# Kernel optimization log

Measured on AMD Instinct MI355X. Metric: run time of the kernel, lower is better.

The kernel has to match this reference:

```python
import jax, jax.numpy as jnp
import numpy as np

B, S, DM, H, HD = 2, 4096, 768, 12, 64
SCALING = HD ** -0.5
LN_EPS = 1e-12
ROPE_BASE = 10000.0


def rotate_half(x):
    x1, x2 = jnp.split(x, 2, axis=-1)
    return jnp.concatenate([-x2, x1], axis=-1)


def setup_inputs() -> dict:
    key = jax.random.key(0)
    ks = jax.random.split(key, 8)
    s = 0.02
    hidden_states = jax.random.normal(ks[0], (B, S, DM), dtype=jnp.float32)
    # true rotary tables: inv_freq over head_dim/2, duplicated (HF convention)
    inv_freq = 1.0 / (ROPE_BASE ** (jnp.arange(0, HD, 2, dtype=jnp.float32) / HD))
    freqs = jnp.arange(S, dtype=jnp.float32)[:, None] * inv_freq[None, :]  # [S, HD/2]
    emb = jnp.concatenate([freqs, freqs], axis=-1)                          # [S, HD]
    cos, sin = jnp.cos(emb), jnp.sin(emb)
    return {
        "hidden_states": hidden_states,
        "cos": cos,
        "sin": sin,
        "Wq": jax.random.normal(ks[1], (DM, DM), dtype=jnp.float32) * s,
        "bq": jnp.zeros((DM,), dtype=jnp.float32),
        "Wk": jax.random.normal(ks[2], (DM, DM), dtype=jnp.float32) * s,
        "bk": jnp.zeros((DM,), dtype=jnp.float32),
        "Wv": jax.random.normal(ks[3], (DM, DM), dtype=jnp.float32) * s,
        "bv": jnp.zeros((DM,), dtype=jnp.float32),
        "Wo": jax.random.normal(ks[4], (DM, DM), dtype=jnp.float32) * s,
        "ln_g": jnp.ones((DM,), dtype=jnp.float32),
        "ln_b": jnp.zeros((DM,), dtype=jnp.float32),
    }


def reference(hidden_states, cos, sin, Wq, bq, Wk, bk, Wv, bv, Wo, ln_g, ln_b):
    # QKV projections -> [B, H, S, HD]
    def proj(W, b):
        return (hidden_states @ W.T + b).reshape(B, S, H, HD).transpose(0, 2, 1, 3)
    q, k, v = proj(Wq, bq), proj(Wk, bk), proj(Wv, bv)

    # RoPE (cos/sin broadcast over batch & heads)
    c = cos[None, None, :, :]
    s_ = sin[None, None, :, :]
    q = q * c + rotate_half(q) * s_
    k = k * c + rotate_half(k) * s_

    # Faithful to source: q pre-scaled, then eager attention scales scores again
    q = q * SCALING
    scores = jnp.einsum("bhsd,bhtd->bhst", q, k) * SCALING  # [B,H,S,S]
    probs = jax.nn.softmax(scores.astype(jnp.float32), axis=-1).astype(v.dtype)
    attn = jnp.einsum("bhst,bhtd->bhsd", probs, v)
    attn = attn.transpose(0, 2, 1, 3).reshape(B, S, DM)

    # output dense (no bias) + residual + LayerNorm
    out = attn @ Wo.T + hidden_states
    mu = jnp.mean(out, axis=-1, keepdims=True)
    var = jnp.var(out, axis=-1, keepdims=True)
    out = (out - mu) * jax.lax.rsqrt(var + LN_EPS) * ln_g + ln_b
    return out
```

## Files before the change

### kernel.cpp

```cpp
#include <hip/hip_runtime.h>
#include <math.h>

#define B_   2
#define S_   4096
#define DM_  768
#define H_   12
#define HD_  64
#define M_   (B_ * S_)
#define ROWELEMS ((size_t)M_ * DM_)
#define WELEMS  ((size_t)DM_ * DM_)

#define QSC (1.4426950408889634f / 64.0f)

typedef unsigned short u16;
typedef unsigned int   u32;
typedef __attribute__((ext_vector_type(8))) short  short8;
typedef __attribute__((ext_vector_type(4))) float  floatx4;
typedef __attribute__((ext_vector_type(4))) u32    uint32x4;

__device__ inline u16 f2bf(float f) {
    u32 u = __builtin_bit_cast(u32, f);
    u += 0x7FFF + ((u >> 16) & 1);
    return (u16)(u >> 16);
}
__device__ inline float bf2f(u16 h) {
    return __builtin_bit_cast(float, (u32)h << 16);
}
__device__ inline u32 pk_trunc(float a, float b) {
    return __builtin_amdgcn_perm(__builtin_bit_cast(u32, b),
                                 __builtin_bit_cast(u32, a), 0x07060302);
}

__device__ inline int sw_off(int r, int cg) {
    return (r << 6) + ((cg ^ (r & 7)) << 3);
}

__device__ __forceinline__ void load_lds16(const u16* g, u16* l) {
    __builtin_amdgcn_global_load_lds(
        (const __attribute__((address_space(1))) u32*)g,
        (__attribute__((address_space(3))) u32*)l, 16, 0, 0);
}

__device__ __forceinline__ void drain_vm() {
    __builtin_amdgcn_s_waitcnt(0x0F70);
}

__global__ __launch_bounds__(256) void conv_bf16(
    const float* __restrict__ h,  const float* __restrict__ wq,
    const float* __restrict__ wk, const float* __restrict__ wv,
    const float* __restrict__ wo, u16* __restrict__ hb, u16* __restrict__ wb)
{
    const int y = blockIdx.y;
    const float* src; u16* dst; size_t n4;
    if (y == 0)      { src = h;  dst = hb;              n4 = ROWELEMS / 4; }
    else if (y == 1) { src = wq; dst = wb;              n4 = WELEMS / 4; }
    else if (y == 2) { src = wk; dst = wb + WELEMS;     n4 = WELEMS / 4; }
    else if (y == 3) { src = wv; dst = wb + 2 * WELEMS; n4 = WELEMS / 4; }
    else             { src = wo; dst = wb + 3 * WELEMS; n4 = WELEMS / 4; }
    const size_t stride = (size_t)gridDim.x * 256;
    for (size_t i = blockIdx.x * 256 + threadIdx.x; i < n4; i += stride) {
        float4 v = *(const float4*)&src[i * 4];
        u32 p0 = (u32)f2bf(v.x) | ((u32)f2bf(v.y) << 16);
        u32 p1 = (u32)f2bf(v.z) | ((u32)f2bf(v.w) << 16);
        *(uint2*)&dst[i * 4] = make_uint2(p0, p1);
    }
}

__global__ __launch_bounds__(256, 3) void gemm_qkv(
    const u16* __restrict__ A,
    const u16* __restrict__ W0, const u16* __restrict__ W1, const u16* __restrict__ W2,
    const float* __restrict__ b0, const float* __restrict__ b1, const float* __restrict__ b2,
    const float* __restrict__ cosT, const float* __restrict__ sinT,
    u16* __restrict__ Qh, u16* __restrict__ Kh, u16* __restrict__ Vt)
{
    __shared__ __align__(16) u16 As[128 * 64];
    __shared__ __align__(16) u16 Ws[128 * 64];

    const int tid  = threadIdx.x;
    const int wave = tid >> 6, lane = tid & 63;
    const int n16  = lane & 15, quad = lane >> 4;
    const int wm   = wave >> 1, wn = wave & 1;
    const int m0   = blockIdx.y * 128, n0 = blockIdx.x * 128;
    const int z    = blockIdx.z;

    const u16* Wz = (z == 0) ? W0 : (z == 1) ? W1 : W2;
    const float* bz = (z == 0) ? b0 : (z == 1) ? b1 : b2;

    int gao[4], ldso[4];
#pragma unroll
    for (int i = 0; i < 4; i++) {
        int g = wave * 256 + i * 64 + lane;
        int r = g >> 3, cg = (g & 7) ^ (r & 7);
        gao[i]  = r * DM_ + cg * 8;
        ldso[i] = (wave * 256 + i * 64) * 8;
    }
    const u16* Ap = A  + (size_t)m0 * DM_;
    const u16* Wp = Wz + (size_t)n0 * DM_;

    floatx4 acc[4][4];
#pragma unroll
    for (int i = 0; i < 4; i++)
#pragma unroll
        for (int j = 0; j < 4; j++) acc[i][j] = (floatx4){0.f, 0.f, 0.f, 0.f};

    for (int k0 = 0; k0 < DM_; k0 += 64) {
        __syncthreads();
#pragma unroll
        for (int i = 0; i < 4; i++) {
            load_lds16(Ap + k0 + gao[i], &As[ldso[i]]);
            load_lds16(Wp + k0 + gao[i], &Ws[ldso[i]]);
        }
        drain_vm();
        __syncthreads();
#pragma unroll
        for (int ks = 0; ks < 2; ks++) {
            short8 af[4], bf[4];
#pragma unroll
            for (int t = 0; t < 4; t++) {
                af[t] = *(const short8*)&As[sw_off(wm * 64 + t * 16 + n16, ks * 4 + quad)];
                bf[t] = *(const short8*)&Ws[sw_off(wn * 64 + t * 16 + n16, ks * 4 + quad)];
            }
#pragma unroll
            for (int i = 0; i < 4; i++)
#pragma unroll
                for (int j = 0; j < 4; j++)
                    acc[i][j] = __builtin_amdgcn_mfma_f32_16x16x32_bf16(
                        af[i], bf[j], acc[i][j], 0, 0, 0);
        }
    }

    if (z == 2) {
#pragma unroll
        for (int i = 0; i < 4; i++)
#pragma unroll
            for (int j = 0; j < 4; j++) {
                const int col = n0 + wn * 64 + j * 16 + n16;
                const int h = col >> 6, hd = col & 63;
                const int row0 = m0 + wm * 64 + i * 16 + quad * 4;
                const int b = row0 >> 12, s0 = row0 & 4095;
                const float bias = bz[col];
                float v0 = acc[i][j][0] + bias, v1 = acc[i][j][1] + bias;
                float v2 = acc[i][j][2] + bias, v3 = acc[i][j][3] + bias;
                u32 w0 = (u32)f2bf(v0) | ((u32)f2bf(v1) << 16);
                u32 w1 = (u32)f2bf(v2) | ((u32)f2bf(v3) << 16);
                *(uint2*)&Vt[((size_t)(b * H_ + h) * HD_ + hd) * S_ + s0] = make_uint2(w0, w1);
            }
    } else {
        u32* Out32 = (u32*)((z == 0) ? Qh : Kh);
        const float sc_ = (z == 0) ? QSC : 1.0f;
#pragma unroll
        for (int i = 0; i < 4; i++)
#pragma unroll
            for (int j = 0; j < 2; j++) {
                const int col1 = n0 + wn * 64 + j * 16 + n16;
                const int col2 = col1 + 32;
                const int h = col1 >> 6, hd1 = col1 & 63;
                const float bias1 = bz[col1], bias2 = bz[col2];
#pragma unroll
                for (int r = 0; r < 4; r++) {
                    const int row = m0 + wm * 64 + i * 16 + quad * 4 + r;
                    const int b = row >> 12, s = row & 4095;
                    const float c  = cosT[s * HD_ + hd1];
                    const float sn = sinT[s * HD_ + hd1];
                    const float x1 = acc[i][j][r] + bias1;
                    const float x2 = acc[i][j + 2][r] + bias2;
                    const float y1 = (x1 * c - x2 * sn) * sc_;
                    const float y2 = (x2 * c + x1 * sn) * sc_;
                    Out32[(((size_t)(b * H_ + h) * S_ + s) << 5) + hd1] =
                        (u32)f2bf(y1) | ((u32)f2bf(y2) << 16);
                }
            }
    }
}

__global__ __launch_bounds__(256, 3) void flash_mfma(
    const u16* __restrict__ Qh, const u16* __restrict__ Kh,
    const u16* __restrict__ Vt, u16* __restrict__ O)
{
    __shared__ __align__(16) u16 Ks[64 * 64];
    __shared__ __align__(16) u16 Vs[64 * 64];

    const int tid  = threadIdx.x;
    const int wave = tid >> 6, lane = tid & 63;
    const int n16  = lane & 15, quad = lane >> 4;
    const int qt   = blockIdx.x;
    const int bh   = blockIdx.y;
    const size_t qk_base = (size_t)bh * S_ * HD_;
    const size_t vt_base = (size_t)bh * HD_ * S_;
    const int q0   = qt * 128;
    const int wrow = wave * 32;

    short8 qf[2][2];
#pragma unroll
    for (int rt = 0; rt < 2; rt++)
#pragma unroll
        for (int ks = 0; ks < 2; ks++)
            qf[rt][ks] = *(const short8*)&Qh[qk_base +
                (size_t)(q0 + wrow + rt * 16 + n16) * HD_ + ks * 32 + quad * 8];

    short8 ones;
#pragma unroll
    for (int j = 0; j < 8; j++) ones[j] = (short)0x3F80;

    int gk_off[2], gv_off[2], ldso[2];
#pragma unroll
    for (int i = 0; i < 2; i++) {
        int g = wave * 128 + i * 64 + lane;
        int r = g >> 3, cg = (g & 7) ^ (r & 7);
        int rk = (r & 0x23) | ((r & 8) << 1) | ((r & 4) << 1) | ((r & 16) >> 2);
        gk_off[i] = rk * HD_ + cg * 8;
        gv_off[i] = r  * S_  + cg * 8;
        ldso[i]   = (wave * 128 + i * 64) * 8;
    }

    floatx4 o_acc[2][4];
    floatx4 o_l[2];
#pragma unroll
    for (int rt = 0; rt < 2; rt++) {
        o_l[rt] = (floatx4){0.f, 0.f, 0.f, 0.f};
#pragma unroll
        for (int dt = 0; dt < 4; dt++) o_acc[rt][dt] = (floatx4){0.f, 0.f, 0.f, 0.f};
    }

    const u16* Kg = Kh + qk_base;
    const u16* Vg = Vt + vt_base;

    for (int kt = 0; kt < 64; kt++) {
        __syncthreads();
#pragma unroll
        for (int i = 0; i < 2; i++) {
            load_lds16(Kg + gk_off[i], &Ks[ldso[i]]);
            load_lds16(Vg + gv_off[i], &Vs[ldso[i]]);
        }
        drain_vm();
        __syncthreads();
        Kg += 64 * HD_;
        Vg += 64;

        floatx4 sct[4][2];
#pragma unroll
        for (int ct = 0; ct < 4; ct++)
#pragma unroll
            for (int rt = 0; rt < 2; rt++)
                sct[ct][rt] = (floatx4){0.f, 0.f, 0.f, 0.f};
#pragma unroll
        for (int ks = 0; ks < 2; ks++) {
            short8 kf[4];
#pragma unroll
            for (int ct = 0; ct < 4; ct++)
                kf[ct] = *(const short8*)&Ks[sw_off(ct * 16 + n16, ks * 4 + quad)];
#pragma unroll
            for (int ct = 0; ct < 4; ct++)
#pragma unroll
                for (int rt = 0; rt < 2; rt++)
                    sct[ct][rt] = __builtin_amdgcn_mfma_f32_16x16x32_bf16(
                        kf[ct], qf[rt][ks], sct[ct][rt], 0, 0, 0);
        }

        short8 pa[2][2];
#pragma unroll
        for (int rt = 0; rt < 2; rt++)
#pragma unroll
            for (int ks = 0; ks < 2; ks++) {
                const floatx4 lo = sct[2 * ks][rt];
                const floatx4 hi = sct[2 * ks + 1][rt];
                uint32x4 w;
                w[0] = pk_trunc(__builtin_amdgcn_exp2f(lo[0]),
                                __builtin_amdgcn_exp2f(lo[1]));
                w[1] = pk_trunc(__builtin_amdgcn_exp2f(lo[2]),
                                __builtin_amdgcn_exp2f(lo[3]));
                w[2] = pk_trunc(__builtin_amdgcn_exp2f(hi[0]),
                                __builtin_amdgcn_exp2f(hi[1]));
                w[3] = pk_trunc(__builtin_amdgcn_exp2f(hi[2]),
                                __builtin_amdgcn_exp2f(hi[3]));
                pa[rt][ks] = __builtin_bit_cast(short8, w);
            }

#pragma unroll
        for (int ks = 0; ks < 2; ks++) {
            short8 vb[4];
#pragma unroll
            for (int dt = 0; dt < 4; dt++)
                vb[dt] = *(const short8*)&Vs[sw_off(dt * 16 + n16, ks * 4 + quad)];
#pragma unroll
            for (int rt = 0; rt < 2; rt++) {
#pragma unroll
                for (int dt = 0; dt < 4; dt++)
                    o_acc[rt][dt] = __builtin_amdgcn_mfma_f32_16x16x32_bf16(
                        pa[rt][ks], vb[dt], o_acc[rt][dt], 0, 0, 0);
                o_l[rt] = __builtin_amdgcn_mfma_f32_16x16x32_bf16(
                    pa[rt][ks], ones, o_l[rt], 0, 0, 0);
            }
        }
    }

    const int b = bh / H_, h = bh % H_;
#pragma unroll
    for (int rt = 0; rt < 2; rt++)
#pragma unroll
        for (int r = 0; r < 4; r++) {
            const float inv = 1.0f / o_l[rt][r];
            const int srow = q0 + wrow + rt * 16 + quad * 4 + r;
            u16* Orow = O + ((size_t)b * S_ + srow) * DM_ + h * HD_;
#pragma unroll
            for (int dt = 0; dt < 4; dt++)
                Orow[dt * 16 + n16] = f2bf(o_acc[rt][dt][r] * inv);
        }
}

__global__ __launch_bounds__(256, 4) void gemm_out(
    const u16* __restrict__ A, const u16* __restrict__ W,
    const float* __restrict__ resid, float* __restrict__ Cf)
{
    __shared__ __align__(16) u16 As[64 * 64];
    __shared__ __align__(16) u16 Ws[128 * 64];

    const int tid  = threadIdx.x;
    const int wave = tid >> 6, lane = tid & 63;
    const int n16  = lane & 15, quad = lane >> 4;
    const int wm   = wave >> 1, wn = wave & 1;
    const int m0   = blockIdx.y * 64, n0 = blockIdx.x * 128;

    int gwo[4], ldswo[4], gao[2], ldsao[2];
#pragma unroll
    for (int i = 0; i < 4; i++) {
        int g = wave * 256 + i * 64 + lane;
        int r = g >> 3, cg = (g & 7) ^ (r & 7);
        gwo[i]   = r * DM_ + cg * 8;
        ldswo[i] = (wave * 256 + i * 64) * 8;
    }
#pragma unroll
    for (int i = 0; i < 2; i++) {
        int g = wave * 128 + i * 64 + lane;
        int r = g >> 3, cg = (g & 7) ^ (r & 7);
        gao[i]   = r * DM_ + cg * 8;
        ldsao[i] = (wave * 128 + i * 64) * 8;
    }
    const u16* Wp = W + (size_t)n0 * DM_;
    const u16* Ap = A + (size_t)m0 * DM_;

    floatx4 acc[2][4];
#pragma unroll
    for (int i = 0; i < 2; i++)
#pragma unroll
        for (int j = 0; j < 4; j++) acc[i][j] = (floatx4){0.f, 0.f, 0.f, 0.f};

    for (int k0 = 0; k0 < DM_; k0 += 64) {
        __syncthreads();
#pragma unroll
        for (int i = 0; i < 4; i++)
            load_lds16(Wp + k0 + gwo[i], &Ws[ldswo[i]]);
#pragma unroll
        for (int i = 0; i < 2; i++)
            load_lds16(Ap + k0 + gao[i], &As[ldsao[i]]);
        drain_vm();
        __syncthreads();

#pragma unroll
        for (int ks = 0; ks < 2; ks++) {
            short8 af[2], bf[4];
#pragma unroll
            for (int rt = 0; rt < 2; rt++)
                af[rt] = *(const short8*)&As[sw_off(wm * 32 + rt * 16 + n16, ks * 4 + quad)];
#pragma unroll
            for (int ct = 0; ct < 4; ct++)
                bf[ct] = *(const short8*)&Ws[sw_off(wn * 64 + ct * 16 + n16, ks * 4 + quad)];
#pragma unroll
            for (int rt = 0; rt < 2; rt++)
#pragma unroll
                for (int ct = 0; ct < 4; ct++)
                    acc[rt][ct] = __builtin_amdgcn_mfma_f32_16x16x32_bf16(
                        af[rt], bf[ct], acc[rt][ct], 0, 0, 0);
        }
    }

#pragma unroll
    for (int rt = 0; rt < 2; rt++)
#pragma unroll
        for (int ct = 0; ct < 4; ct++) {
            const int col = n0 + wn * 64 + ct * 16 + n16;
#pragma unroll
            for (int r = 0; r < 4; r++) {
                const int row = m0 + wm * 32 + rt * 16 + quad * 4 + r;
                Cf[(size_t)row * DM_ + col] = acc[rt][ct][r] + resid[(size_t)row * DM_ + col];
            }
        }
}

__global__ __launch_bounds__(256) void ln_kernel(
    float* __restrict__ io, const float* __restrict__ g, const float* __restrict__ bb)
{
    const int row = blockIdx.x, t = threadIdx.x;
    float* p = io + (size_t)row * DM_;
    float x[3];
    float sum = 0.0f, sq = 0.0f;
#pragma unroll
    for (int i = 0; i < 3; i++) {
        x[i] = p[t + i * 256];
        sum += x[i];
        sq  = fmaf(x[i], x[i], sq);
    }
#pragma unroll
    for (int off = 32; off >= 1; off >>= 1) {
        sum += __shfl_xor(sum, off);
        sq  += __shfl_xor(sq, off);
    }
    __shared__ float s1[4], s2[4];
    if ((t & 63) == 0) { s1[t >> 6] = sum; s2[t >> 6] = sq; }
    __syncthreads();
    sum = s1[0] + s1[1] + s1[2] + s1[3];
    sq  = s2[0] + s2[1] + s2[2] + s2[3];
    const float mu  = sum * (1.0f / 768.0f);
    const float var = sq * (1.0f / 768.0f) - mu * mu;
    const float rs  = rsqrtf(var + 1e-12f);
#pragma unroll
    for (int i = 0; i < 3; i++) {
        const int c = t + i * 256;
        p[c] = (x[i] - mu) * rs * g[c] + bb[c];
    }
}

extern "C" void kernel_launch(void* const* d_in, const int* in_sizes, int n_in,
                              void* d_out, int out_size, void* d_ws, size_t ws_size,
                              hipStream_t stream)
{
    const float* hidden = (const float*)d_in[0];
    const float* cosT   = (const float*)d_in[1];
    const float* sinT   = (const float*)d_in[2];
    const float* Wq     = (const float*)d_in[3];
    const float* bq     = (const float*)d_in[4];
    const float* Wk     = (const float*)d_in[5];
    const float* bk     = (const float*)d_in[6];
    const float* Wv     = (const float*)d_in[7];
    const float* bv     = (const float*)d_in[8];
    const float* Wo     = (const float*)d_in[9];
    const float* ln_g   = (const float*)d_in[10];
    const float* ln_b   = (const float*)d_in[11];
    float* out = (float*)d_out;

    u16* wsb = (u16*)d_ws;
    u16* Hb  = wsb;
    u16* Wb  = wsb + ROWELEMS;
    u16* Qh  = Wb + 4 * WELEMS;
    u16* Kh  = Qh + ROWELEMS;
    u16* Vt  = Kh + ROWELEMS;
    u16* Ob  = Hb;
    u16* Wqb = Wb, *Wkb = Wb + WELEMS, *Wvb = Wb + 2 * WELEMS, *Wob = Wb + 3 * WELEMS;

    conv_bf16<<<dim3(1024, 5), 256, 0, stream>>>(hidden, Wq, Wk, Wv, Wo, Hb, Wb);

    gemm_qkv<<<dim3(DM_ / 128, M_ / 128, 3), 256, 0, stream>>>(
        Hb, Wqb, Wkb, Wvb, bq, bk, bv, cosT, sinT, Qh, Kh, Vt);

    flash_mfma<<<dim3(S_ / 128, B_ * H_), 256, 0, stream>>>(Qh, Kh, Vt, Ob);

    gemm_out<<<dim3(DM_ / 128, M_ / 64), 256, 0, stream>>>(Ob, Wob, hidden, out);

    ln_kernel<<<M_, 256, 0, stream>>>(out, ln_g, ln_b);
}
```

Before: 269.1 us.

## Split KV range across wave pairs in flash attention with LDS reduction

```diff
diff --git a/kernel.cpp b/kernel.cpp
--- a/kernel.cpp
+++ b/kernel.cpp
@@ -173,30 +173,30 @@
     }
 }
 
-__global__ __launch_bounds__(256, 3) void flash_mfma(
+__global__ __launch_bounds__(256, 2) void flash_mfma(
     const u16* __restrict__ Qh, const u16* __restrict__ Kh,
     const u16* __restrict__ Vt, u16* __restrict__ O)
 {
-    __shared__ __align__(16) u16 Ks[64 * 64];
-    __shared__ __align__(16) u16 Vs[64 * 64];
+    __shared__ __align__(16) u16 SMEM[16640];
 
     const int tid  = threadIdx.x;
     const int wave = tid >> 6, lane = tid & 63;
     const int n16  = lane & 15, quad = lane >> 4;
+    const int kvh  = wave & 1;
+    const int qh   = wave >> 1;
     const int qt   = blockIdx.x;
     const int bh   = blockIdx.y;
     const size_t qk_base = (size_t)bh * S_ * HD_;
     const size_t vt_base = (size_t)bh * HD_ * S_;
     const int q0   = qt * 128;
-    const int wrow = wave * 32;
-
-    short8 qf[2][2];
-#pragma unroll
-    for (int rt = 0; rt < 2; rt++)
+
+    short8 qf[4][2];
+#pragma unroll
+    for (int rt = 0; rt < 4; rt++)
 #pragma unroll
         for (int ks = 0; ks < 2; ks++)
             qf[rt][ks] = *(const short8*)&Qh[qk_base +
-                (size_t)(q0 + wrow + rt * 16 + n16) * HD_ + ks * 32 + quad * 8];
+                (size_t)(q0 + qh * 64 + rt * 16 + n16) * HD_ + ks * 32 + quad * 8];
 
     short8 ones;
 #pragma unroll
@@ -213,10 +213,10 @@
         ldso[i]   = (wave * 128 + i * 64) * 8;
     }
 
-    floatx4 o_acc[2][4];
-    floatx4 o_l[2];
-#pragma unroll
-    for (int rt = 0; rt < 2; rt++) {
+    floatx4 o_acc[4][4];
+    floatx4 o_l[4];
+#pragma unroll
+    for (int rt = 0; rt < 4; rt++) {
         o_l[rt] = (floatx4){0.f, 0.f, 0.f, 0.f};
 #pragma unroll
         for (int dt = 0; dt < 4; dt++) o_acc[rt][dt] = (floatx4){0.f, 0.f, 0.f, 0.f};
@@ -225,41 +225,46 @@
     const u16* Kg = Kh + qk_base;
     const u16* Vg = Vt + vt_base;
 
-    for (int kt = 0; kt < 64; kt++) {
+    u16* Ksb = &SMEM[kvh * 8192];
+    u16* Vsb = &SMEM[kvh * 8192 + 4096];
+
+    for (int it = 0; it < 32; it++) {
         __syncthreads();
 #pragma unroll
         for (int i = 0; i < 2; i++) {
-            load_lds16(Kg + gk_off[i], &Ks[ldso[i]]);
-            load_lds16(Vg + gv_off[i], &Vs[ldso[i]]);
+            load_lds16(Kg + gk_off[i],               &SMEM[ldso[i]]);
+            load_lds16(Vg + gv_off[i],               &SMEM[4096  + ldso[i]]);
+            load_lds16(Kg + 32 * 64 * HD_ + gk_off[i], &SMEM[8192  + ldso[i]]);
+            load_lds16(Vg + 32 * 64 + gv_off[i],     &SMEM[12288 + ldso[i]]);
         }
         drain_vm();
         __syncthreads();
         Kg += 64 * HD_;
         Vg += 64;
 
-        floatx4 sct[4][2];
+        floatx4 sct[4][4];
 #pragma unroll
         for (int ct = 0; ct < 4; ct++)
 #pragma unroll
-            for (int rt = 0; rt < 2; rt++)
+            for (int rt = 0; rt < 4; rt++)
                 sct[ct][rt] = (floatx4){0.f, 0.f, 0.f, 0.f};
 #pragma unroll
         for (int ks = 0; ks < 2; ks++) {
             short8 kf[4];
 #pragma unroll
             for (int ct = 0; ct < 4; ct++)
-                kf[ct] = *(const short8*)&Ks[sw_off(ct * 16 + n16, ks * 4 + quad)];
+                kf[ct] = *(const short8*)&Ksb[sw_off(ct * 16 + n16, ks * 4 + quad)];
 #pragma unroll
             for (int ct = 0; ct < 4; ct++)
 #pragma unroll
-                for (int rt = 0; rt < 2; rt++)
+                for (int rt = 0; rt < 4; rt++)
                     sct[ct][rt] = __builtin_amdgcn_mfma_f32_16x16x32_bf16(
                         kf[ct], qf[rt][ks], sct[ct][rt], 0, 0, 0);
         }
 
-        short8 pa[2][2];
-#pragma unroll
-        for (int rt = 0; rt < 2; rt++)
+        short8 pa[4][2];
+#pragma unroll
+        for (int rt = 0; rt < 4; rt++)
 #pragma unroll
             for (int ks = 0; ks < 2; ks++) {
                 const floatx4 lo = sct[2 * ks][rt];
@@ -281,9 +286,9 @@
             short8 vb[4];
 #pragma unroll
             for (int dt = 0; dt < 4; dt++)
-                vb[dt] = *(const short8*)&Vs[sw_off(dt * 16 + n16, ks * 4 + quad)];
-#pragma unroll
-            for (int rt = 0; rt < 2; rt++) {
+                vb[dt] = *(const short8*)&Vsb[sw_off(dt * 16 + n16, ks * 4 + quad)];
+#pragma unroll
+            for (int rt = 0; rt < 4; rt++) {
 #pragma unroll
                 for (int dt = 0; dt < 4; dt++)
                     o_acc[rt][dt] = __builtin_amdgcn_mfma_f32_16x16x32_bf16(
@@ -294,18 +299,41 @@
         }
     }
 
-    const int b = bh / H_, h = bh % H_;
-#pragma unroll
-    for (int rt = 0; rt < 2; rt++)
-#pragma unroll
-        for (int r = 0; r < 4; r++) {
-            const float inv = 1.0f / o_l[rt][r];
-            const int srow = q0 + wrow + rt * 16 + quad * 4 + r;
-            u16* Orow = O + ((size_t)b * S_ + srow) * DM_ + h * HD_;
-#pragma unroll
-            for (int dt = 0; dt < 4; dt++)
-                Orow[dt * 16 + n16] = f2bf(o_acc[rt][dt][r] * inv);
-        }
+    __syncthreads();
+    float* Op = (float*)SMEM;
+    float* lp = (float*)&SMEM[16384];
+    if (kvh == 1) {
+#pragma unroll
+        for (int rt = 0; rt < 4; rt++)
+#pragma unroll
+            for (int r = 0; r < 4; r++) {
+                const int row = rt * 16 + quad * 4 + r;
+                if (n16 == 0) lp[qh * 64 + row] = o_l[rt][r];
+#pragma unroll
+                for (int dt = 0; dt < 4; dt++)
+                    Op[qh * 4096 + row * 64 + dt * 16 + n16] = o_acc[rt][dt][r];
+            }
+    }
+    __syncthreads();
+    if (kvh == 0) {
+        const int b = bh / H_, h = bh % H_;
+#pragma unroll
+        for (int rt = 0; rt < 4; rt++)
+#pragma unroll
+            for (int r = 0; r < 4; r++) {
+                const int row = rt * 16 + quad * 4 + r;
+                const float lsum = o_l[rt][r] + lp[qh * 64 + row];
+                const float inv  = 1.0f / lsum;
+                const int srow = q0 + qh * 64 + row;
+                u16* Orow = O + ((size_t)b * S_ + srow) * DM_ + h * HD_;
+#pragma unroll
+                for (int dt = 0; dt < 4; dt++) {
+                    const float v = o_acc[rt][dt][r] +
+                                    Op[qh * 4096 + row * 64 + dt * 16 + n16];
+                    Orow[dt * 16 + n16] = f2bf(v * inv);
+                }
+            }
+    }
 }
 
 __global__ __launch_bounds__(256, 4) void gemm_out(
```

Measured after the change: 295.3 us. 1.1x slower.

## Double-buffer K/V LDS tiles in flash attention to overlap loads with compute

Applied to the files above, without the earlier changes.

```diff
diff --git a/kernel.cpp b/kernel.cpp
--- a/kernel.cpp
+++ b/kernel.cpp
@@ -43,6 +43,9 @@
 
 __device__ __forceinline__ void drain_vm() {
     __builtin_amdgcn_s_waitcnt(0x0F70);
+}
+__device__ __forceinline__ void wait_vm4() {
+    __builtin_amdgcn_s_waitcnt(0x0F74);
 }
 
 __global__ __launch_bounds__(256) void conv_bf16(
@@ -177,8 +180,10 @@
     const u16* __restrict__ Qh, const u16* __restrict__ Kh,
     const u16* __restrict__ Vt, u16* __restrict__ O)
 {
-    __shared__ __align__(16) u16 Ks[64 * 64];
-    __shared__ __align__(16) u16 Vs[64 * 64];
+    __shared__ __align__(16) u16 Ks0[64 * 64];
+    __shared__ __align__(16) u16 Vs0[64 * 64];
+    __shared__ __align__(16) u16 Ks1[64 * 64];
+    __shared__ __align__(16) u16 Vs1[64 * 64];
 
     const int tid  = threadIdx.x;
     const int wave = tid >> 6, lane = tid & 63;
@@ -225,74 +230,98 @@
     const u16* Kg = Kh + qk_base;
     const u16* Vg = Vt + vt_base;
 
-    for (int kt = 0; kt < 64; kt++) {
-        __syncthreads();
-#pragma unroll
-        for (int i = 0; i < 2; i++) {
-            load_lds16(Kg + gk_off[i], &Ks[ldso[i]]);
-            load_lds16(Vg + gv_off[i], &Vs[ldso[i]]);
-        }
-        drain_vm();
-        __syncthreads();
-        Kg += 64 * HD_;
-        Vg += 64;
-
-        floatx4 sct[4][2];
-#pragma unroll
-        for (int ct = 0; ct < 4; ct++)
-#pragma unroll
-            for (int rt = 0; rt < 2; rt++)
-                sct[ct][rt] = (floatx4){0.f, 0.f, 0.f, 0.f};
-#pragma unroll
-        for (int ks = 0; ks < 2; ks++) {
-            short8 kf[4];
-#pragma unroll
-            for (int ct = 0; ct < 4; ct++)
-                kf[ct] = *(const short8*)&Ks[sw_off(ct * 16 + n16, ks * 4 + quad)];
-#pragma unroll
-            for (int ct = 0; ct < 4; ct++)
-#pragma unroll
-                for (int rt = 0; rt < 2; rt++)
-                    sct[ct][rt] = __builtin_amdgcn_mfma_f32_16x16x32_bf16(
-                        kf[ct], qf[rt][ks], sct[ct][rt], 0, 0, 0);
-        }
-
-        short8 pa[2][2];
-#pragma unroll
-        for (int rt = 0; rt < 2; rt++)
-#pragma unroll
-            for (int ks = 0; ks < 2; ks++) {
-                const floatx4 lo = sct[2 * ks][rt];
-                const floatx4 hi = sct[2 * ks + 1][rt];
-                uint32x4 w;
-                w[0] = pk_trunc(__builtin_amdgcn_exp2f(lo[0]),
-                                __builtin_amdgcn_exp2f(lo[1]));
-                w[1] = pk_trunc(__builtin_amdgcn_exp2f(lo[2]),
-                                __builtin_amdgcn_exp2f(lo[3]));
-                w[2] = pk_trunc(__builtin_amdgcn_exp2f(hi[0]),
-                                __builtin_amdgcn_exp2f(hi[1]));
-                w[3] = pk_trunc(__builtin_amdgcn_exp2f(hi[2]),
-                                __builtin_amdgcn_exp2f(hi[3]));
-                pa[rt][ks] = __builtin_bit_cast(short8, w);
-            }
-
-#pragma unroll
-        for (int ks = 0; ks < 2; ks++) {
-            short8 vb[4];
-#pragma unroll
-            for (int dt = 0; dt < 4; dt++)
-                vb[dt] = *(const short8*)&Vs[sw_off(dt * 16 + n16, ks * 4 + quad)];
-#pragma unroll
-            for (int rt = 0; rt < 2; rt++) {
-#pragma unroll
-                for (int dt = 0; dt < 4; dt++)
-                    o_acc[rt][dt] = __builtin_amdgcn_mfma_f32_16x16x32_bf16(
-                        pa[rt][ks], vb[dt], o_acc[rt][dt], 0, 0, 0);
-                o_l[rt] = __builtin_amdgcn_mfma_f32_16x16x32_bf16(
-                    pa[rt][ks], ones, o_l[rt], 0, 0, 0);
-            }
-        }
-    }
+#define STAGE(KSRC, VSRC, KDST, VDST)                                   \
+    do {                                                                \
+        _Pragma("unroll")                                               \
+        for (int i_ = 0; i_ < 2; i_++) {                                \
+            load_lds16((KSRC) + gk_off[i_], &(KDST)[ldso[i_]]);         \
+            load_lds16((VSRC) + gv_off[i_], &(VDST)[ldso[i_]]);         \
+        }                                                               \
+    } while (0)
+
+#define COMPUTE_TILE(KSB, VSB)                                          \
+    do {                                                                \
+        floatx4 sct[4][2];                                              \
+        _Pragma("unroll")                                               \
+        for (int ct = 0; ct < 4; ct++)                                  \
+            _Pragma("unroll")                                           \
+            for (int rt = 0; rt < 2; rt++)                              \
+                sct[ct][rt] = (floatx4){0.f, 0.f, 0.f, 0.f};            \
+        _Pragma("unroll")                                               \
+        for (int ks = 0; ks < 2; ks++) {                                \
+            short8 kf[4];                                               \
+            _Pragma("unroll")                                           \
+            for (int ct = 0; ct < 4; ct++)                              \
+                kf[ct] = *(const short8*)&(KSB)[sw_off(ct * 16 + n16,   \
+                                                       ks * 4 + quad)]; \
+            _Pragma("unroll")                                           \
+            for (int ct = 0; ct < 4; ct++)                              \
+                _Pragma("unroll")                                       \
+                for (int rt = 0; rt < 2; rt++)                          \
+                    sct[ct][rt] = __builtin_amdgcn_mfma_f32_16x16x32_bf16( \
+                        kf[ct], qf[rt][ks], sct[ct][rt], 0, 0, 0);      \
+        }                                                               \
+        short8 pa[2][2];                                                \
+        _Pragma("unroll")                                               \
+        for (int rt = 0; rt < 2; rt++)                                  \
+            _Pragma("unroll")                                           \
+            for (int ks = 0; ks < 2; ks++) {                            \
+                const floatx4 lo = sct[2 * ks][rt];                     \
+                const floatx4 hi = sct[2 * ks + 1][rt];                 \
+                uint32x4 w;                                             \
+                w[0] = pk_trunc(__builtin_amdgcn_exp2f(lo[0]),          \
+                                __builtin_amdgcn_exp2f(lo[1]));         \
+                w[1] = pk_trunc(__builtin_amdgcn_exp2f(lo[2]),          \
+                                __builtin_amdgcn_exp2f(lo[3]));         \
+                w[2] = pk_trunc(__builtin_amdgcn_exp2f(hi[0]),          \
+                                __builtin_amdgcn_exp2f(hi[1]));         \
+                w[3] = pk_trunc(__builtin_amdgcn_exp2f(hi[2]),          \
+                                __builtin_amdgcn_exp2f(hi[3]));         \
+                pa[rt][ks] = __builtin_bit_cast(short8, w);             \
+            }                                                           \
+        _Pragma("unroll")                                               \
+        for (int ks = 0; ks < 2; ks++) {                                \
+            short8 vb[4];                                               \
+            _Pragma("unroll")                                           \
+            for (int dt = 0; dt < 4; dt++)                              \
+                vb[dt] = *(const short8*)&(VSB)[sw_off(dt * 16 + n16,   \
+                                                       ks * 4 + quad)]; \
+            _Pragma("unroll")                                           \
+            for (int rt = 0; rt < 2; rt++) {                            \
+                _Pragma("unroll")                                       \
+                for (int dt = 0; dt < 4; dt++)                          \
+                    o_acc[rt][dt] = __builtin_amdgcn_mfma_f32_16x16x32_bf16( \
+                        pa[rt][ks], vb[dt], o_acc[rt][dt], 0, 0, 0);    \
+                o_l[rt] = __builtin_amdgcn_mfma_f32_16x16x32_bf16(      \
+                    pa[rt][ks], ones, o_l[rt], 0, 0, 0);                \
+            }                                                           \
+        }                                                               \
+    } while (0)
+
+    STAGE(Kg, Vg, Ks0, Vs0);
+
+    for (int kt = 0; kt < 64; kt += 2) {
+        STAGE(Kg + 64 * HD_, Vg + 64, Ks1, Vs1);
+        wait_vm4();
+        __builtin_amdgcn_s_barrier();
+        COMPUTE_TILE(Ks0, Vs0);
+        __builtin_amdgcn_s_barrier();
+
+        if (kt + 2 < 64) {
+            STAGE(Kg + 2 * 64 * HD_, Vg + 2 * 64, Ks0, Vs0);
+            wait_vm4();
+        } else {
+            drain_vm();
+        }
+        __builtin_amdgcn_s_barrier();
+        COMPUTE_TILE(Ks1, Vs1);
+        __builtin_amdgcn_s_barrier();
+
+        Kg += 2 * 64 * HD_;
+        Vg += 2 * 64;
+    }
+#undef STAGE
+#undef COMPUTE_TILE
 
     const int b = bh / H_, h = bh % H_;
 #pragma unroll
```

Result: slower. 280.5 us (+4.2%).
